# Kernel optimization log

Hardware: AMD Instinct MI355X
Metric: run time of the kernel (lower is better)

## Reference

```python
import jax, jax.numpy as jnp
import numpy as np

N = 20000   # nodes
E = 160000  # edges (avg degree 8)
D = 128     # hidden_dim
H1 = 8      # heads for conv1/conv2
H3 = 4      # final_heads for conv3
SLOPE = 0.2 # GATv2 leaky_relu negative slope (PyG default)


def setup_inputs() -> dict:
    key = jax.random.key(0)
    ks = jax.random.split(key, 16)
    x = jax.random.normal(ks[0], (N, D), jnp.float32)
    # edges with src != dst (PyG removes self loops then re-adds them)
    src = jax.random.randint(ks[1], (E,), 0, N, dtype=jnp.int32)
    off = jax.random.randint(ks[2], (E,), 1, N, dtype=jnp.int32)
    dst = (src + off) % N
    edge_index = jnp.stack([src, dst])  # [2, E] int32

    def lin(k, h):
        return jax.random.normal(k, (D, h * D), jnp.float32) * (1.0 / np.sqrt(D))

    def attv(k, h):
        return jax.random.normal(k, (h, D), jnp.float32) * (1.0 / np.sqrt(D))

    return {
        'x': x, 'edge_index': edge_index,
        'Wl1': lin(ks[3], H1), 'Wr1': lin(ks[4], H1), 'att1': attv(ks[5], H1), 'b1': jnp.zeros((D,), jnp.float32),
        'Wl2': lin(ks[6], H1), 'Wr2': lin(ks[7], H1), 'att2': attv(ks[8], H1), 'b2': jnp.zeros((D,), jnp.float32),
        'Wl3': lin(ks[9], H3), 'Wr3': lin(ks[10], H3), 'att3': attv(ks[11], H3), 'b3': jnp.zeros((D,), jnp.float32),
    }


def gatv2_layer(x, src, dst, Wl, Wr, att, b):
    """One GATv2Conv (share_weights=False, concat=False -> head mean, bias)."""
    n = x.shape[0]
    H, C = att.shape
    xl = (x @ Wl).reshape(n, H, C)  # source-side transform (messages)
    xr = (x @ Wr).reshape(n, H, C)  # target-side transform
    z = jax.nn.leaky_relu(xl[src] + xr[dst], SLOPE)        # [Etot, H, C]
    e = jnp.einsum('ehc,hc->eh', z, att)                   # [Etot, H]
    # per-destination segment softmax over incoming edges
    m = jax.ops.segment_max(e, dst, num_segments=n)        # [N, H]
    a = jnp.exp(e - m[dst])
    s = jax.ops.segment_sum(a, dst, num_segments=n)
    alpha = a / s[dst]                                     # [Etot, H]
    out = jax.ops.segment_sum(xl[src] * alpha[..., None], dst, num_segments=n)  # [N, H, C]
    return out.mean(axis=1) + b


def reference(x, edge_index, Wl1, Wr1, att1, b1, Wl2, Wr2, att2, b2, Wl3, Wr3, att3, b3):
    n = x.shape[0]
    loops = jnp.arange(n, dtype=edge_index.dtype)  # add_self_loops=True
    src = jnp.concatenate([edge_index[0], loops])
    dst = jnp.concatenate([edge_index[1], loops])
    h = x
    h = jax.nn.relu(gatv2_layer(h, src, dst, Wl1, Wr1, att1, b1)) + h
    h = jax.nn.relu(gatv2_layer(h, src, dst, Wl2, Wr2, att2, b2)) + h
    h = gatv2_layer(h, src, dst, Wl3, Wr3, att3, b3) + h
    return h
```

## Files before the change

### kernel.cpp

```cpp
#include <hip/hip_runtime.h>
#include <math.h>

#define NN 20000
#define NE 160000
#define DH 128

typedef _Float16 f16;
typedef f16 f16x2 __attribute__((ext_vector_type(2)));
typedef f16 f16x4 __attribute__((ext_vector_type(4)));
typedef f16 f16x8 __attribute__((ext_vector_type(8)));
typedef float f32x4 __attribute__((ext_vector_type(4)));
typedef unsigned int uint32;
typedef unsigned char u8;

__global__ void conv_count_kernel(const float* __restrict__ X, f16* __restrict__ XH,
                                  int n4, const int* __restrict__ edst,
                                  int* __restrict__ deg, int ne) {
  int i = blockIdx.x * blockDim.x + threadIdx.x;
  if (i < n4) {
    float4 v = *(const float4*)(X + (size_t)i * 4);
    f16x4 o = {(f16)v.x, (f16)v.y, (f16)v.z, (f16)v.w};
    *(f16x4*)(XH + (size_t)i * 4) = o;
  }
  if (i < ne) atomicAdd(&deg[edst[i]], 1);
}

__global__ __launch_bounds__(1024) void csr_p1(const int* __restrict__ deg,
                                               int* __restrict__ rowstart,
                                               int* __restrict__ bsum,
                                               int* __restrict__ ghist, int n) {
  __shared__ int wsum[16];
  __shared__ int lhist[64];
  const int tid = threadIdx.x;
  const int lane = tid & 63, w = tid >> 6;
  if (tid < 64) lhist[tid] = 0;
  __syncthreads();
  int i = blockIdx.x * 1024 + tid;
  int d = (i < n) ? deg[i] : 0;
  if (i < n) atomicAdd(&lhist[d < 63 ? d : 63], 1);
  int v = d;
#pragma unroll
  for (int off = 1; off < 64; off <<= 1) {
    int u = __shfl_up(v, off, 64);
    if (lane >= off) v += u;
  }
  if (lane == 63) wsum[w] = v;
  __syncthreads();
  if (w == 0) {
    int t = (lane < 16) ? wsum[lane] : 0;
#pragma unroll
    for (int off = 1; off < 16; off <<= 1) {
      int u = __shfl_up(t, off, 64);
      if (lane >= off) t += u;
    }
    if (lane < 16) wsum[lane] = t;
  }
  __syncthreads();
  int add = (w > 0 ? wsum[w - 1] : 0);
  if (i < n) rowstart[i + 1] = v + add;
  if (tid == 0) bsum[blockIdx.x] = wsum[15];
  if (tid < 64) ghist[blockIdx.x * 64 + tid] = lhist[tid];
}

__global__ __launch_bounds__(1024) void csr_p3(const int* __restrict__ deg,
                                               int* __restrict__ rowstart,
                                               const int* __restrict__ bsum,
                                               const int* __restrict__ ghist,
                                               int* __restrict__ perm, int n, int nb) {
  __shared__ int lcur[64];
  __shared__ int base[64];
  __shared__ int radd_s;
  const int tid = threadIdx.x;
  if (tid < 64) {
    lcur[tid] = 0;
    int pre = 0, tot = 0;
    for (int b = 0; b < nb; b++) {
      int v = ghist[b * 64 + tid];
      pre += (b < (int)blockIdx.x) ? v : 0;
      tot += v;
    }
    int incl = tot;
#pragma unroll
    for (int off = 1; off < 64; off <<= 1) {
      int u = __shfl_up(incl, off, 64);
      if (tid >= off) incl += u;
    }
    base[tid] = (n - incl) + pre;
  }
  if (tid == 0) {
    int r = 0;
    for (int b = 0; b < (int)blockIdx.x; b++) r += bsum[b];
    radd_s = r;
  }
  __syncthreads();
  int i = blockIdx.x * 1024 + tid;
  if (i < n) {
    rowstart[i + 1] += radd_s;
    int d = deg[i];
    int b = d < 63 ? d : 63;
    int pos = atomicAdd(&lcur[b], 1);
    perm[base[b] + pos] = i;
  }
  if (blockIdx.x == 0 && tid == 0) rowstart[0] = 0;
}

__global__ void scatter_kernel(const int* __restrict__ src, const int* __restrict__ dstp,
                               const int* __restrict__ rowstart, int* __restrict__ cursor,
                               int* __restrict__ csr, int n) {
  int i = blockIdx.x * blockDim.x + threadIdx.x;
  if (i < n) {
    int d = dstp[i];
    int pos = atomicAdd(&cursor[d], 1);
    csr[rowstart[d] + pos] = src[i];
  }
}

__global__ void sort_kernel(const int* __restrict__ rowstart, int* __restrict__ csr,
                            const int* __restrict__ perm, int n) {
  int idx = blockIdx.x * blockDim.x + threadIdx.x;
  int sub = idx >> 4;
  int u = idx & 15;
  if (sub >= n) return;
  int i = perm[sub];
  int a = rowstart[i], b = rowstart[i + 1];
  int d = b - a;
  if (d <= 1) return;
  if (d <= 16) {
    int v = (u < d) ? csr[a + u] : 0x7FFFFFFF;
#pragma unroll
    for (int k = 2; k <= 16; k <<= 1) {
#pragma unroll
      for (int j = 16; j > 0; j >>= 1) {
        if (j > (k >> 1)) continue;
        int o = __shfl_xor(v, j, 64);
        bool takeMin = (((u & k) == 0) == ((u & j) == 0));
        v = takeMin ? (v < o ? v : o) : (v > o ? v : o);
      }
    }
    if (u < d) csr[a + u] = v;
  } else if (u == 0) {
    for (int j = a + 1; j < b; j++) {
      int v = csr[j];
      int k = j - 1;
      while (k >= a && csr[k] > v) { csr[k + 1] = csr[k]; k--; }
      csr[k + 1] = v;
    }
  }
}

__global__ __launch_bounds__(256) void transconv_all(
    const float* __restrict__ W0, const float* __restrict__ W1,
    const float* __restrict__ W2, const float* __restrict__ W3,
    const float* __restrict__ W4, const float* __restrict__ W5,
    f16* O0, f16* O1, f16* O2, f16* O3, f16* O4, f16* O5) {
  const float* W; f16* O; int HC;
  switch (blockIdx.z) {
    case 0: W = W0; O = O0; HC = 1024; break;
    case 1: W = W1; O = O1; HC = 1024; break;
    case 2: W = W2; O = O2; HC = 1024; break;
    case 3: W = W3; O = O3; HC = 1024; break;
    case 4: W = W4; O = O4; HC = 512; break;
    default: W = W5; O = O5; HC = 512; break;
  }
  int c0 = blockIdx.x * 32;
  if (c0 >= HC) return;
  __shared__ float t[32][33];
  int k0 = blockIdx.y * 32;
  int tx = threadIdx.x & 31, ty = threadIdx.x >> 5;
#pragma unroll
  for (int j = 0; j < 4; j++) {
    int k = k0 + ty + j * 8;
    t[ty + j * 8][tx] = W[(size_t)k * HC + c0 + tx];
  }
  __syncthreads();
#pragma unroll
  for (int j = 0; j < 4; j++) {
    int c = c0 + ty + j * 8;
    O[(size_t)c * 128 + k0 + tx] = (f16)t[tx][ty + j * 8];
  }
}

template <int YB>
__global__ __launch_bounds__(256) void gemm_f16(const f16* __restrict__ A,
                                                const f16* __restrict__ BT,
                                                f16* __restrict__ C, int M, int Nout) {
  const int nx = (M + 127) / 128;
  const int chunk = nx * YB / 8;
  const int bid = blockIdx.x;
  const int p = (bid % 8) * chunk + bid / 8;
  const int bx = p / YB, by = p % YB;

  const int w = threadIdx.x >> 6, lane = threadIdx.x & 63;
  const int wm = w >> 1, wn = w & 1;
  const int row0 = bx * 128 + wm * 64;
  const int col0 = by * 128 + wn * 64;
  const int lr = lane & 15, lk = (lane >> 4) * 8;

  __shared__ f16 ct[128][144];

  f32x4 acc[4][4] = {};
  const f16* Arow[4];
  const f16* Brow[4];
#pragma unroll
  for (int m = 0; m < 4; m++) {
    int r = row0 + m * 16 + lr;
    r = r < M ? r : M - 1;
    Arow[m] = A + (size_t)r * 128 + lk;
  }
#pragma unroll
  for (int n = 0; n < 4; n++) {
    int c = col0 + n * 16 + lr;
    Brow[n] = BT + (size_t)c * 128 + lk;
  }
#pragma unroll
  for (int ks = 0; ks < 4; ks++) {
    f16x8 a[4], b[4];
#pragma unroll
    for (int m = 0; m < 4; m++) a[m] = *(const f16x8*)(Arow[m] + ks * 32);
#pragma unroll
    for (int n = 0; n < 4; n++) b[n] = *(const f16x8*)(Brow[n] + ks * 32);
#pragma unroll
    for (int m = 0; m < 4; m++)
#pragma unroll
      for (int n = 0; n < 4; n++)
        acc[m][n] = __builtin_amdgcn_mfma_f32_16x16x32_f16(a[m], b[n], acc[m][n], 0, 0, 0);
  }
  const int lrow = wm * 64, lcol = wn * 64;
#pragma unroll
  for (int m = 0; m < 4; m++) {
    int rbase = lrow + m * 16 + (lane >> 4) * 4;
#pragma unroll
    for (int r = 0; r < 4; r++) {
#pragma unroll
      for (int n = 0; n < 4; n++) {
        ct[rbase + r][lcol + n * 16 + lr] = (f16)acc[m][n][r];
      }
    }
  }
  __syncthreads();
  const int t = threadIdx.x;
  const int cidx = (t & 15) * 8;
  const int rowblk = bx * 128, colblk = by * 128;
#pragma unroll
  for (int rr = (t >> 4); rr < 128; rr += 16) {
    int gr = rowblk + rr;
    if (gr < M) {
      uint4 v = *(const uint4*)(&ct[rr][cidx]);
      *(uint4*)(C + (size_t)gr * Nout + colblk + cidx) = v;
    }
  }
}

template <int YB>
__global__ __launch_bounds__(256) void gemm_f16_split(const f16* __restrict__ A,
                                                      const f16* __restrict__ BT,
                                                      u8* __restrict__ C8,
                                                      f16* __restrict__ C16, int M) {
  const int Nout = YB * 128;
  const int nx = (M + 127) / 128;
  const int chunk = nx * YB / 8;
  const int bid = blockIdx.x;
  const int p = (bid % 8) * chunk + bid / 8;
  const int bx = p / YB, by = p % YB;

  const int w = threadIdx.x >> 6, lane = threadIdx.x & 63;
  const int wm = w >> 1, wn = w & 1;
  const int row0 = bx * 128 + wm * 64;
  const int col0 = by * 128 + wn * 64;
  const int lr = lane & 15, lk = (lane >> 4) * 8;

  __shared__ f16 ct[128][144];

  f32x4 acc[4][4] = {};
  const f16* Arow[4];
  const f16* Brow[4];
#pragma unroll
  for (int m = 0; m < 4; m++) {
    int r = row0 + m * 16 + lr;
    r = r < M ? r : M - 1;
    Arow[m] = A + (size_t)r * 128 + lk;
  }
#pragma unroll
  for (int n = 0; n < 4; n++) {
    int c = col0 + n * 16 + lr;
    Brow[n] = BT + (size_t)c * 128 + lk;
  }
#pragma unroll
  for (int ks = 0; ks < 4; ks++) {
    f16x8 a[4], b[4];
#pragma unroll
    for (int m = 0; m < 4; m++) a[m] = *(const f16x8*)(Arow[m] + ks * 32);
#pragma unroll
    for (int n = 0; n < 4; n++) b[n] = *(const f16x8*)(Brow[n] + ks * 32);
#pragma unroll
    for (int m = 0; m < 4; m++)
#pragma unroll
      for (int n = 0; n < 4; n++)
        acc[m][n] = __builtin_amdgcn_mfma_f32_16x16x32_f16(a[m], b[n], acc[m][n], 0, 0, 0);
  }
  const int lrow = wm * 64, lcol = wn * 64;
#pragma unroll
  for (int m = 0; m < 4; m++) {
    int rbase = lrow + m * 16 + (lane >> 4) * 4;
#pragma unroll
    for (int r = 0; r < 4; r++) {
#pragma unroll
      for (int n = 0; n < 4; n++) {
        ct[rbase + r][lcol + n * 16 + lr] = (f16)acc[m][n][r];
      }
    }
  }
  __syncthreads();
  const int t = threadIdx.x;
  const int cidx = (t & 15) * 8;
  const int rowblk = bx * 128, colblk = by * 128;
  if (by < YB / 2) {
#pragma unroll
    for (int rr = (t >> 4); rr < 128; rr += 16) {
      int gr = rowblk + rr;
      if (gr < M) {
        f16x8 v = *(const f16x8*)(&ct[rr][cidx]);
        int lo = __builtin_amdgcn_cvt_pk_fp8_f32((float)v[0], (float)v[1], 0, false);
        lo = __builtin_amdgcn_cvt_pk_fp8_f32((float)v[2], (float)v[3], lo, true);
        int hi = __builtin_amdgcn_cvt_pk_fp8_f32((float)v[4], (float)v[5], 0, false);
        hi = __builtin_amdgcn_cvt_pk_fp8_f32((float)v[6], (float)v[7], hi, true);
        uint2 o;
        o.x = (uint32)lo;
        o.y = (uint32)hi;
        *(uint2*)(C8 + (size_t)gr * 1024 + colblk + cidx) = o;
      }
    }
  } else {
    const int col16 = colblk - 1024;
#pragma unroll
    for (int rr = (t >> 4); rr < 128; rr += 16) {
      int gr = rowblk + rr;
      if (gr < M) {
        uint4 v = *(const uint4*)(&ct[rr][cidx]);
        *(uint4*)(C16 + (size_t)gr * 1024 + col16 + cidx) = v;
      }
    }
  }
}

struct LV { f16x2 v[4]; };

__device__ __forceinline__ f16x2 bc2(uint32 x) { return __builtin_bit_cast(f16x2, x); }

__device__ __forceinline__ LV load8(const char* __restrict__ base, uint32 off) {
  uint4 r = *(const uint4*)(base + off);
  LV o;
  o.v[0] = bc2(r.x); o.v[1] = bc2(r.y); o.v[2] = bc2(r.z); o.v[3] = bc2(r.w);
  return o;
}

__device__ __forceinline__ LV load8_f8(const char* __restrict__ base, uint32 off) {
  uint2 w = *(const uint2*)(base + off);
  auto a = __builtin_amdgcn_cvt_pk_f32_fp8((int)w.x, false);
  auto b = __builtin_amdgcn_cvt_pk_f32_fp8((int)w.x, true);
  auto c = __builtin_amdgcn_cvt_pk_f32_fp8((int)w.y, false);
  auto d = __builtin_amdgcn_cvt_pk_f32_fp8((int)w.y, true);
  LV o;
  o.v[0] = __builtin_bit_cast(f16x2, __builtin_amdgcn_cvt_pkrtz(a[0], a[1]));
  o.v[1] = __builtin_bit_cast(f16x2, __builtin_amdgcn_cvt_pkrtz(b[0], b[1]));
  o.v[2] = __builtin_bit_cast(f16x2, __builtin_amdgcn_cvt_pkrtz(c[0], c[1]));
  o.v[3] = __builtin_bit_cast(f16x2, __builtin_amdgcn_cvt_pkrtz(d[0], d[1]));
  return o;
}

template <bool F8>
__device__ __forceinline__ LV loadxl(const char* __restrict__ p, uint32 off) {
  if constexpr (F8) return load8_f8(p, off);
  else return load8(p, off);
}

__device__ __forceinline__ f16x2 leaky2(f16x2 z) {
  f16x2 zs = z * (f16)0.2f;
  return __builtin_elementwise_max(z, zs);
}

__device__ __forceinline__ float edot(const LV& x, const f16x2* xr2, const f16x2* att2) {
  float ea = 0.f, eb = 0.f;
  ea = __builtin_amdgcn_fdot2(leaky2(x.v[0] + xr2[0]), att2[0], ea, false);
  eb = __builtin_amdgcn_fdot2(leaky2(x.v[1] + xr2[1]), att2[1], eb, false);
  ea = __builtin_amdgcn_fdot2(leaky2(x.v[2] + xr2[2]), att2[2], ea, false);
  eb = __builtin_amdgcn_fdot2(leaky2(x.v[3] + xr2[3]), att2[3], eb, false);
  return ea + eb;
}

template <int PAT>
__device__ __forceinline__ float swz(float x) {
  return __int_as_float(__builtin_amdgcn_ds_swizzle(__float_as_int(x), PAT));
}

__device__ __forceinline__ void red16x4(float& a, float& b, float& c, float& d) {
  a += swz<0x041F>(a); b += swz<0x041F>(b); c += swz<0x041F>(c); d += swz<0x041F>(d);
  a += swz<0x081F>(a); b += swz<0x081F>(b); c += swz<0x081F>(c); d += swz<0x081F>(d);
  a += swz<0x101F>(a); b += swz<0x101F>(b); c += swz<0x101F>(c); d += swz<0x101F>(d);
  a += swz<0x201F>(a); b += swz<0x201F>(b); c += swz<0x201F>(c); d += swz<0x201F>(d);
}
__device__ __forceinline__ float red16(float a) {
  a += swz<0x041F>(a);
  a += swz<0x081F>(a);
  a += swz<0x101F>(a);
  a += swz<0x201F>(a);
  return a;
}

template <int H, int DG, bool RELU, bool WF32, bool F8, int LGXL, int LGXR>
__global__ __launch_bounds__(H * DG * 64) void agg_kernel(
    const f16* __restrict__ h_in, const char* __restrict__ xlp,
    const char* __restrict__ xrp, const float* __restrict__ att,
    const float* __restrict__ bias, const int* __restrict__ csr,
    const int* __restrict__ rowstart, const int* __restrict__ perm,
    float* __restrict__ h_out, f16* __restrict__ hh) {
  __shared__ float headout[H][4 * DG][DH];
  __shared__ int nodes[4 * DG];
  const int wv = threadIdx.x >> 6;
  const int h = wv & (H - 1);
  const int dg = wv / H;
  const int lane = threadIdx.x & 63;
  const int g = lane >> 4, u = lane & 15;
  const int c0 = u * 8;
  if (threadIdx.x < 4 * DG) nodes[threadIdx.x] = perm[blockIdx.x * 4 * DG + threadIdx.x];
  const int dst = perm[blockIdx.x * 4 * DG + dg * 4 + g];
  const uint32 loff_xl = (uint32)(h * DH + c0) << (F8 ? 0 : 1);
  const uint32 loff_xr = (uint32)(h * DH + c0) * 2;

  f16x2 att2[4], xr2[4];
  {
    const float* ap = att + h * DH + c0;
    float a0[8];
    *(float4*)a0 = *(const float4*)ap;
    *(float4*)(a0 + 4) = *(const float4*)(ap + 4);
#pragma unroll
    for (int q = 0; q < 4; q++) att2[q] = f16x2{(f16)a0[2 * q], (f16)a0[2 * q + 1]};
    LV xrv = load8(xrp, ((uint32)dst << LGXR) + loff_xr);
#pragma unroll
    for (int q = 0; q < 4; q++) xr2[q] = xrv.v[q];
  }

  const int js = rowstart[dst], je = rowstart[dst + 1];

  float m, s;
  f16x2 acc[4];
  {
    LV xv = loadxl<F8>(xlp, ((uint32)dst << LGXL) + loff_xl);
    m = red16(edot(xv, xr2, att2));
    s = 1.f;
#pragma unroll
    for (int q = 0; q < 4; q++) acc[q] = xv.v[q];
  }

  LV pf0, pf1, pf2, pf3;
  {
    int ja = js < je ? js : je - 1;
    int jb = js + 1 < je ? js + 1 : je - 1;
    int jc = js + 2 < je ? js + 2 : je - 1;
    int jd = js + 3 < je ? js + 3 : je - 1;
    if (js < je) {
      pf0 = loadxl<F8>(xlp, ((uint32)csr[ja] << LGXL) + loff_xl);
      pf1 = loadxl<F8>(xlp, ((uint32)csr[jb] << LGXL) + loff_xl);
      pf2 = loadxl<F8>(xlp, ((uint32)csr[jc] << LGXL) + loff_xl);
      pf3 = loadxl<F8>(xlp, ((uint32)csr[jd] << LGXL) + loff_xl);
    }
  }

  int j = js;
  for (; j + 3 < je; j += 4) {
    LV cv0 = pf0, cv1 = pf1, cv2 = pf2, cv3 = pf3;
    int ja = j + 4 < je ? j + 4 : je - 1;
    int jb = j + 5 < je ? j + 5 : je - 1;
    int jc = j + 6 < je ? j + 6 : je - 1;
    int jd = j + 7 < je ? j + 7 : je - 1;
    pf0 = loadxl<F8>(xlp, ((uint32)csr[ja] << LGXL) + loff_xl);
    pf1 = loadxl<F8>(xlp, ((uint32)csr[jb] << LGXL) + loff_xl);
    pf2 = loadxl<F8>(xlp, ((uint32)csr[jc] << LGXL) + loff_xl);
    pf3 = loadxl<F8>(xlp, ((uint32)csr[jd] << LGXL) + loff_xl);

    float e0 = edot(cv0, xr2, att2);
    float e1 = edot(cv1, xr2, att2);
    float e2 = edot(cv2, xr2, att2);
    float e3 = edot(cv3, xr2, att2);
    red16x4(e0, e1, e2, e3);

    float mn = fmaxf(fmaxf(fmaxf(m, e0), fmaxf(e1, e2)), e3);
    float a = __expf(m - mn);
    float p0 = __expf(e0 - mn);
    float p1 = __expf(e1 - mn);
    float p2 = __expf(e2 - mn);
    float p3 = __expf(e3 - mn);
    s = s * a + ((p0 + p1) + (p2 + p3));
    f16 ah = (f16)a, g0 = (f16)p0, g1 = (f16)p1, g2 = (f16)p2, g3 = (f16)p3;
    f16x2 a2 = {ah, ah}, q0 = {g0, g0}, q1 = {g1, g1}, q2 = {g2, g2}, q3 = {g3, g3};
#pragma unroll
    for (int q = 0; q < 4; q++) {
      f16x2 t = acc[q] * a2;
      t = cv0.v[q] * q0 + t;
      t = cv1.v[q] * q1 + t;
      t = cv2.v[q] * q2 + t;
      t = cv3.v[q] * q3 + t;
      acc[q] = t;
    }
    m = mn;
  }
  for (int t = 0; j < je; j++, t++) {
    LV cv = (t == 0) ? pf0 : (t == 1) ? pf1 : pf2;
    float e = red16(edot(cv, xr2, att2));
    float mn = fmaxf(m, e);
    float a = __expf(m - mn);
    float p = __expf(e - mn);
    s = s * a + p;
    f16 ah = (f16)a, gh = (f16)p;
    f16x2 a2 = {ah, ah}, p2 = {gh, gh};
#pragma unroll
    for (int q = 0; q < 4; q++) acc[q] = acc[q] * a2 + cv.v[q] * p2;
    m = mn;
  }

  float inv = 1.f / s;
#pragma unroll
  for (int q = 0; q < 4; q++) {
    headout[h][dg * 4 + g][c0 + 2 * q] = (float)acc[q][0] * inv;
    headout[h][dg * 4 + g][c0 + 2 * q + 1] = (float)acc[q][1] * inv;
  }
  __syncthreads();
  for (int t = threadIdx.x; t < 4 * DG * DH; t += H * DG * 64) {
    int d = t >> 7, c = t & 127;
    float sum = 0.f;
#pragma unroll
    for (int q = 0; q < H; q++) sum += headout[q][d][c];
    float r = sum * (1.f / H) + bias[c];
    if (RELU) r = fmaxf(r, 0.f);
    int node = nodes[d];
    float o = r + (float)h_in[(size_t)node * DH + c];
    if (WF32) h_out[(size_t)node * DH + c] = o;
    else hh[(size_t)node * DH + c] = (f16)o;
  }
}

extern "C" void kernel_launch(void* const* d_in, const int* in_sizes, int n_in,
                              void* d_out, int out_size, void* d_ws, size_t ws_size,
                              hipStream_t stream) {
  const float* x = (const float*)d_in[0];
  const int* ei = (const int*)d_in[1];
  const float* Wl1 = (const float*)d_in[2];
  const float* Wr1 = (const float*)d_in[3];
  const float* att1 = (const float*)d_in[4];
  const float* b1 = (const float*)d_in[5];
  const float* Wl2 = (const float*)d_in[6];
  const float* Wr2 = (const float*)d_in[7];
  const float* att2 = (const float*)d_in[8];
  const float* b2 = (const float*)d_in[9];
  const float* Wl3 = (const float*)d_in[10];
  const float* Wr3 = (const float*)d_in[11];
  const float* att3 = (const float*)d_in[12];
  const float* b3 = (const float*)d_in[13];
  float* out = (float*)d_out;

  char* p = (char*)d_ws;
  f16* xlr = (f16*)p; p += (size_t)NN * 2048 * 2;
  u8* xl8  = (u8*)p;  p += (size_t)NN * 1024;
  f16* xh  = (f16*)p; p += (size_t)NN * DH * 2;
  f16* h1h = (f16*)p; p += (size_t)NN * DH * 2;
  f16* h2h = (f16*)p; p += (size_t)NN * DH * 2;
  f16* WT1 = (f16*)p; p += (size_t)2048 * 128 * 2;
  f16* WT2 = (f16*)p; p += (size_t)2048 * 128 * 2;
  f16* WT3 = (f16*)p; p += (size_t)1024 * 128 * 2;
  int* deg      = (int*)p; p += (size_t)NN * 4;
  int* cursor   = (int*)p; p += (size_t)NN * 4;
  int* rowstart = (int*)p; p += (size_t)(NN + 1) * 4;
  int* perm     = (int*)p; p += (size_t)NN * 4;
  int* bsum     = (int*)p; p += (size_t)32 * 4;
  int* ghist    = (int*)p; p += (size_t)20 * 64 * 4;
  int* csr      = (int*)p;

  const int* esrc = ei;
  const int* edst = ei + NE;

  const int nbc = (NN + 1023) / 1024;

  hipMemsetAsync(deg, 0, sizeof(int) * 2 * NN, stream);
  conv_count_kernel<<<(NN * DH / 4 + 255) / 256, 256, 0, stream>>>(
      x, xh, NN * DH / 4, edst, deg, NE);
  csr_p1<<<nbc, 1024, 0, stream>>>(deg, rowstart, bsum, ghist, NN);
  csr_p3<<<nbc, 1024, 0, stream>>>(deg, rowstart, bsum, ghist, perm, NN, nbc);
  scatter_kernel<<<(NE + 255) / 256, 256, 0, stream>>>(esrc, edst, rowstart, cursor, csr, NE);
  sort_kernel<<<(NN * 16 + 255) / 256, 256, 0, stream>>>(rowstart, csr, perm, NN);
  transconv_all<<<dim3(32, 4, 6), 256, 0, stream>>>(
      Wl1, Wr1, Wl2, Wr2, Wl3, Wr3,
      WT1, WT1 + (size_t)1024 * 128, WT2, WT2 + (size_t)1024 * 128,
      WT3, WT3 + (size_t)512 * 128);

  const int nx = (NN + 127) / 128;

  gemm_f16_split<16><<<nx * 16, 256, 0, stream>>>(xh, WT1, xl8, xlr, NN);
  agg_kernel<8, 1, true, false, true, 10, 11><<<NN / 4, 512, 0, stream>>>(
      xh, (const char*)xl8, (const char*)xlr, att1, b1, csr, rowstart, perm,
      nullptr, h1h);
  gemm_f16<16><<<nx * 16, 256, 0, stream>>>(h1h, WT2, xlr, NN, 2048);
  agg_kernel<8, 1, true, false, false, 12, 12><<<NN / 4, 512, 0, stream>>>(
      h1h, (const char*)xlr, (const char*)xlr + 2048, att2, b2, csr, rowstart,
      perm, nullptr, h2h);
  gemm_f16<8><<<nx * 8, 256, 0, stream>>>(h2h, WT3, xlr, NN, 1024);
  agg_kernel<4, 2, false, true, false, 11, 11><<<NN / 8, 512, 0, stream>>>(
      h2h, (const char*)xlr, (const char*)xlr + 1024, att3, b3, csr, rowstart,
      perm, out, nullptr);
}
```

Measured before the change: 312.0 us.

## Store both xl and xr in fp8 for layers one and two, halve epilogue LDS

```diff
diff --git a/kernel.cpp b/kernel.cpp
--- a/kernel.cpp
+++ b/kernel.cpp
@@ -180,15 +180,17 @@
   }
 }
 
+
 template <int YB>
-__global__ __launch_bounds__(256) void gemm_f16(const f16* __restrict__ A,
-                                                const f16* __restrict__ BT,
-                                                f16* __restrict__ C, int M, int Nout) {
+__device__ __forceinline__ void gemm_core(const f16* __restrict__ A,
+                                          const f16* __restrict__ BT, int M,
+                                          int& bx, int& by, f32x4 (&acc)[4][4]) {
   const int nx = (M + 127) / 128;
   const int chunk = nx * YB / 8;
   const int bid = blockIdx.x;
   const int p = (bid % 8) * chunk + bid / 8;
-  const int bx = p / YB, by = p % YB;
+  bx = p / YB;
+  by = p % YB;
 
   const int w = threadIdx.x >> 6, lane = threadIdx.x & 63;
   const int wm = w >> 1, wn = w & 1;
@@ -196,9 +198,6 @@
   const int col0 = by * 128 + wn * 64;
   const int lr = lane & 15, lk = (lane >> 4) * 8;
 
-  __shared__ f16 ct[128][144];
-
-  f32x4 acc[4][4] = {};
   const f16* Arow[4];
   const f16* Brow[4];
 #pragma unroll
@@ -225,99 +224,85 @@
       for (int n = 0; n < 4; n++)
         acc[m][n] = __builtin_amdgcn_mfma_f32_16x16x32_f16(a[m], b[n], acc[m][n], 0, 0, 0);
   }
-  const int lrow = wm * 64, lcol = wn * 64;
-#pragma unroll
-  for (int m = 0; m < 4; m++) {
-    int rbase = lrow + m * 16 + (lane >> 4) * 4;
-#pragma unroll
-    for (int r = 0; r < 4; r++) {
-#pragma unroll
-      for (int n = 0; n < 4; n++) {
-        ct[rbase + r][lcol + n * 16 + lr] = (f16)acc[m][n][r];
-      }
-    }
-  }
-  __syncthreads();
+}
+
+template <int YB>
+__global__ __launch_bounds__(256) void gemm_f16(const f16* __restrict__ A,
+                                                const f16* __restrict__ BT,
+                                                f16* __restrict__ C, int M, int Nout) {
+  __shared__ f16 ct[64][144];
+  int bx, by;
+  f32x4 acc[4][4] = {};
+  gemm_core<YB>(A, BT, M, bx, by, acc);
+
+  const int w = threadIdx.x >> 6, lane = threadIdx.x & 63;
+  const int wm = w >> 1, wn = w & 1;
+  const int lr = lane & 15;
+  const int lcol = wn * 64;
   const int t = threadIdx.x;
   const int cidx = (t & 15) * 8;
   const int rowblk = bx * 128, colblk = by * 128;
-#pragma unroll
-  for (int rr = (t >> 4); rr < 128; rr += 16) {
-    int gr = rowblk + rr;
-    if (gr < M) {
-      uint4 v = *(const uint4*)(&ct[rr][cidx]);
-      *(uint4*)(C + (size_t)gr * Nout + colblk + cidx) = v;
-    }
+
+#pragma unroll
+  for (int half = 0; half < 2; half++) {
+    if (wm == half) {
+#pragma unroll
+      for (int m = 0; m < 4; m++) {
+        int rbase = m * 16 + (lane >> 4) * 4;
+#pragma unroll
+        for (int r = 0; r < 4; r++)
+#pragma unroll
+          for (int n = 0; n < 4; n++)
+            ct[rbase + r][lcol + n * 16 + lr] = (f16)acc[m][n][r];
+      }
+    }
+    __syncthreads();
+#pragma unroll
+    for (int rr = (t >> 4); rr < 64; rr += 16) {
+      int gr = rowblk + half * 64 + rr;
+      if (gr < M) {
+        uint4 v = *(const uint4*)(&ct[rr][cidx]);
+        *(uint4*)(C + (size_t)gr * Nout + colblk + cidx) = v;
+      }
+    }
+    __syncthreads();
   }
 }
 
 template <int YB>
-__global__ __launch_bounds__(256) void gemm_f16_split(const f16* __restrict__ A,
-                                                      const f16* __restrict__ BT,
-                                                      u8* __restrict__ C8,
-                                                      f16* __restrict__ C16, int M) {
-  const int Nout = YB * 128;
-  const int nx = (M + 127) / 128;
-  const int chunk = nx * YB / 8;
-  const int bid = blockIdx.x;
-  const int p = (bid % 8) * chunk + bid / 8;
-  const int bx = p / YB, by = p % YB;
+__global__ __launch_bounds__(256) void gemm_f8(const f16* __restrict__ A,
+                                               const f16* __restrict__ BT,
+                                               u8* __restrict__ C8, int M) {
+  __shared__ f16 ct[64][144];
+  int bx, by;
+  f32x4 acc[4][4] = {};
+  gemm_core<YB>(A, BT, M, bx, by, acc);
 
   const int w = threadIdx.x >> 6, lane = threadIdx.x & 63;
   const int wm = w >> 1, wn = w & 1;
-  const int row0 = bx * 128 + wm * 64;
-  const int col0 = by * 128 + wn * 64;
-  const int lr = lane & 15, lk = (lane >> 4) * 8;
-
-  __shared__ f16 ct[128][144];
-
-  f32x4 acc[4][4] = {};
-  const f16* Arow[4];
-  const f16* Brow[4];
-#pragma unroll
-  for (int m = 0; m < 4; m++) {
-    int r = row0 + m * 16 + lr;
-    r = r < M ? r : M - 1;
-    Arow[m] = A + (size_t)r * 128 + lk;
-  }
-#pragma unroll
-  for (int n = 0; n < 4; n++) {
-    int c = col0 + n * 16 + lr;
-    Brow[n] = BT + (size_t)c * 128 + lk;
-  }
-#pragma unroll
-  for (int ks = 0; ks < 4; ks++) {
-    f16x8 a[4], b[4];
-#pragma unroll
-    for (int m = 0; m < 4; m++) a[m] = *(const f16x8*)(Arow[m] + ks * 32);
-#pragma unroll
-    for (int n = 0; n < 4; n++) b[n] = *(const f16x8*)(Brow[n] + ks * 32);
-#pragma unroll
-    for (int m = 0; m < 4; m++)
-#pragma unroll
-      for (int n = 0; n < 4; n++)
-        acc[m][n] = __builtin_amdgcn_mfma_f32_16x16x32_f16(a[m], b[n], acc[m][n], 0, 0, 0);
-  }
-  const int lrow = wm * 64, lcol = wn * 64;
-#pragma unroll
-  for (int m = 0; m < 4; m++) {
-    int rbase = lrow + m * 16 + (lane >> 4) * 4;
-#pragma unroll
-    for (int r = 0; r < 4; r++) {
-#pragma unroll
-      for (int n = 0; n < 4; n++) {
-        ct[rbase + r][lcol + n * 16 + lr] = (f16)acc[m][n][r];
-      }
-    }
-  }
-  __syncthreads();
+  const int lr = lane & 15;
+  const int lcol = wn * 64;
   const int t = threadIdx.x;
   const int cidx = (t & 15) * 8;
   const int rowblk = bx * 128, colblk = by * 128;
-  if (by < YB / 2) {
-#pragma unroll
-    for (int rr = (t >> 4); rr < 128; rr += 16) {
-      int gr = rowblk + rr;
+
+#pragma unroll
+  for (int half = 0; half < 2; half++) {
+    if (wm == half) {
+#pragma unroll
+      for (int m = 0; m < 4; m++) {
+        int rbase = m * 16 + (lane >> 4) * 4;
+#pragma unroll
+        for (int r = 0; r < 4; r++)
+#pragma unroll
+          for (int n = 0; n < 4; n++)
+            ct[rbase + r][lcol + n * 16 + lr] = (f16)acc[m][n][r];
+      }
+    }
+    __syncthreads();
+#pragma unroll
+    for (int rr = (t >> 4); rr < 64; rr += 16) {
+      int gr = rowblk + half * 64 + rr;
       if (gr < M) {
         f16x8 v = *(const f16x8*)(&ct[rr][cidx]);
         int lo = __builtin_amdgcn_cvt_pk_fp8_f32((float)v[0], (float)v[1], 0, false);
@@ -327,19 +312,10 @@
         uint2 o;
         o.x = (uint32)lo;
         o.y = (uint32)hi;
-        *(uint2*)(C8 + (size_t)gr * 1024 + colblk + cidx) = o;
+        *(uint2*)(C8 + (size_t)gr * 2048 + colblk + cidx) = o;
       }
     }
-  } else {
-    const int col16 = colblk - 1024;
-#pragma unroll
-    for (int rr = (t >> 4); rr < 128; rr += 16) {
-      int gr = rowblk + rr;
-      if (gr < M) {
-        uint4 v = *(const uint4*)(&ct[rr][cidx]);
-        *(uint4*)(C16 + (size_t)gr * 1024 + col16 + cidx) = v;
-      }
-    }
+    __syncthreads();
   }
 }
 
@@ -407,7 +383,7 @@
   return a;
 }
 
-template <int H, int DG, bool RELU, bool WF32, bool F8, int LGXL, int LGXR>
+template <int H, int DG, bool RELU, bool WF32, bool F8, bool XR8, int LGXL, int LGXR>
 __global__ __launch_bounds__(H * DG * 64) void agg_kernel(
     const f16* __restrict__ h_in, const char* __restrict__ xlp,
     const char* __restrict__ xrp, const float* __restrict__ att,
@@ -425,7 +401,7 @@
   if (threadIdx.x < 4 * DG) nodes[threadIdx.x] = perm[blockIdx.x * 4 * DG + threadIdx.x];
   const int dst = perm[blockIdx.x * 4 * DG + dg * 4 + g];
   const uint32 loff_xl = (uint32)(h * DH + c0) << (F8 ? 0 : 1);
-  const uint32 loff_xr = (uint32)(h * DH + c0) * 2;
+  const uint32 loff_xr = (uint32)(h * DH + c0) << (XR8 ? 0 : 1);
 
   f16x2 att2[4], xr2[4];
   {
@@ -435,7 +411,7 @@
     *(float4*)(a0 + 4) = *(const float4*)(ap + 4);
 #pragma unroll
     for (int q = 0; q < 4; q++) att2[q] = f16x2{(f16)a0[2 * q], (f16)a0[2 * q + 1]};
-    LV xrv = load8(xrp, ((uint32)dst << LGXR) + loff_xr);
+    LV xrv = loadxl<XR8>(xrp, ((uint32)dst << LGXR) + loff_xr);
 #pragma unroll
     for (int q = 0; q < 4; q++) xr2[q] = xrv.v[q];
   }
@@ -560,7 +536,7 @@
 
   char* p = (char*)d_ws;
   f16* xlr = (f16*)p; p += (size_t)NN * 2048 * 2;
-  u8* xl8  = (u8*)p;  p += (size_t)NN * 1024;
+  u8* xl8  = (u8*)p;  p += (size_t)NN * 2048;
   f16* xh  = (f16*)p; p += (size_t)NN * DH * 2;
   f16* h1h = (f16*)p; p += (size_t)NN * DH * 2;
   f16* h2h = (f16*)p; p += (size_t)NN * DH * 2;
@@ -594,16 +570,16 @@
 
   const int nx = (NN + 127) / 128;
 
-  gemm_f16_split<16><<<nx * 16, 256, 0, stream>>>(xh, WT1, xl8, xlr, NN);
-  agg_kernel<8, 1, true, false, true, 10, 11><<<NN / 4, 512, 0, stream>>>(
-      xh, (const char*)xl8, (const char*)xlr, att1, b1, csr, rowstart, perm,
-      nullptr, h1h);
-  gemm_f16<16><<<nx * 16, 256, 0, stream>>>(h1h, WT2, xlr, NN, 2048);
-  agg_kernel<8, 1, true, false, false, 12, 12><<<NN / 4, 512, 0, stream>>>(
-      h1h, (const char*)xlr, (const char*)xlr + 2048, att2, b2, csr, rowstart,
+  gemm_f8<16><<<nx * 16, 256, 0, stream>>>(xh, WT1, xl8, NN);
+  agg_kernel<8, 1, true, false, true, true, 11, 11><<<NN / 4, 512, 0, stream>>>(
+      xh, (const char*)xl8, (const char*)xl8 + 1024, att1, b1, csr, rowstart,
+      perm, nullptr, h1h);
+  gemm_f8<16><<<nx * 16, 256, 0, stream>>>(h1h, WT2, xl8, NN);
+  agg_kernel<8, 1, true, false, true, true, 11, 11><<<NN / 4, 512, 0, stream>>>(
+      h1h, (const char*)xl8, (const char*)xl8 + 1024, att2, b2, csr, rowstart,
       perm, nullptr, h2h);
   gemm_f16<8><<<nx * 8, 256, 0, stream>>>(h2h, WT3, xlr, NN, 1024);
-  agg_kernel<4, 2, false, true, false, 11, 11><<<NN / 8, 512, 0, stream>>>(
+  agg_kernel<4, 2, false, true, false, false, 11, 11><<<NN / 8, 512, 0, stream>>>(
       h2h, (const char*)xlr, (const char*)xlr + 1024, att3, b3, csr, rowstart,
       perm, out, nullptr);
 }
```

Result: faster. 302.2 us (-3.1%).
